# Kernel optimization log

Measured on AMD Instinct MI355X. Metric: run time of the kernel, lower is better.

Reference implementation:

```python
import jax, jax.numpy as jnp
import numpy as np

EPS = 1e-5


def _conv_w(x, k):
    # cross-correlation along width, kernel size 2, padding 1 -> width W+1
    xp = jnp.pad(x, ((0, 0), (0, 0), (0, 0), (1, 1)))
    return k[0] * xp[..., :-1] + k[1] * xp[..., 1:]


def _conv_h(x, k):
    # cross-correlation along height, kernel size 2, padding 1 -> height H+1
    xp = jnp.pad(x, ((0, 0), (0, 0), (1, 1), (0, 0)))
    return k[0] * xp[..., :-1, :] + k[1] * xp[..., 1:, :]


def _dwt(x, lp, hp):
    L = _conv_h(_conv_w(x, lp), lp)
    Hc = _conv_h(_conv_w(x, hp), hp)
    return L[:, :, ::2, ::2], Hc[:, :, ::2, ::2]


def _bn(y, g, b, m, v):
    # eval-mode batchnorm over channel axis 1
    scale = (g / jnp.sqrt(v + EPS))[None, :, None, None]
    shift = (b - m * g / jnp.sqrt(v + EPS))[None, :, None, None]
    return y * scale + shift


def setup_inputs() -> dict:
    key = jax.random.key(0)
    ks = jax.random.split(key, 8)
    S, B, H, W, C = 5, 8, 512, 512, 64
    x = jax.random.normal(ks[0], (B, 1, H, W), dtype=jnp.float32)
    lp = jnp.tile(jnp.array([0.7071, 0.7071], dtype=jnp.float32), (S, 1))
    hp = jnp.tile(jnp.array([0.7071, -0.7071], dtype=jnp.float32), (S, 1))
    w1 = jax.random.normal(ks[1], (S, C, 1), dtype=jnp.float32) * 0.5
    w2 = jax.random.normal(ks[2], (S, C, C), dtype=jnp.float32) * (1.0 / np.sqrt(C))
    g1 = jnp.ones((S, C), jnp.float32)
    b1 = jnp.zeros((S, C), jnp.float32)
    m1 = jax.random.normal(ks[3], (S, C), dtype=jnp.float32) * 0.1
    v1 = jax.random.uniform(ks[4], (S, C), dtype=jnp.float32) + 0.5
    g2 = jnp.ones((S, C), jnp.float32)
    b2 = jnp.zeros((S, C), jnp.float32)
    m2 = jax.random.normal(ks[5], (S, C), dtype=jnp.float32) * 0.1
    v2 = jax.random.uniform(ks[6], (S, C), dtype=jnp.float32) + 0.5
    return dict(x=x, lp=lp, hp=hp, w1=w1, w2=w2, g1=g1, b1=b1, m1=m1, v1=v1,
                g2=g2, b2=b2, m2=m2, v2=v2)


def reference(x, lp, hp, w1, w2, g1, b1, m1, v1, g2, b2, m2, v2):
    # Returns stacked-over-scale (L, H_coeff, processed_L):
    #   L, Hc: [S, B, 1, H', W'];  P: [S, B, 64, H', W']
    def per_scale(lp_s, hp_s, w1_s, g1_s, b1_s, m1_s, v1_s,
                  w2_s, g2_s, b2_s, m2_s, v2_s):
        L, Hc = _dwt(x, lp_s, hp_s)
        y = jnp.einsum('oc,bchw->bohw', w1_s, L)
        y = jax.nn.relu(_bn(y, g1_s, b1_s, m1_s, v1_s))
        y = jnp.einsum('oc,bchw->bohw', w2_s, y)
        y = jax.nn.relu(_bn(y, g2_s, b2_s, m2_s, v2_s))
        return L, Hc, y

    return jax.vmap(per_scale)(lp, hp, w1, g1, b1, m1, v1, w2, g2, b2, m2, v2)
```

## Files before the change

kernel.cpp:

```cpp
#include <hip/hip_runtime.h>
#include <math.h>

#define EPSF 1e-5f

constexpr int Sn = 5, Bn = 8, Hin = 512, Win = 512, Cn = 64;
constexpr int HO = 257, WO = 257;
constexpr int HW = HO * WO;
constexpr int NPIX = Bn * HW;
constexpr int TOTPIX = Sn * NPIX;

constexpr int WSF = 64 + Cn * 66 * 2;

__global__ __launch_bounds__(64) void precompute_kernel(
    const float* __restrict__ w1, const float* __restrict__ w2,
    const float* __restrict__ g1, const float* __restrict__ b1,
    const float* __restrict__ m1, const float* __restrict__ v1,
    const float* __restrict__ g2, const float* __restrict__ b2,
    const float* __restrict__ m2, const float* __restrict__ v2,
    float* __restrict__ ws) {
    int s = blockIdx.x;
    int c = threadIdx.x;
    __shared__ float sa1[Cn], st1[Cn], stc[Cn], stS[Cn];
    __shared__ int   scS[Cn];

    int idx = s * Cn + c;
    float sc1 = g1[idx] / sqrtf(v1[idx] + EPSF);
    float a1  = sc1 * w1[idx];
    float t1  = b1[idx] - m1[idx] * sc1;
    sa1[c] = a1;
    st1[c] = t1;
    float tc = (a1 != 0.f) ? (-t1 / a1) : INFINITY;
    stc[c] = tc;
    __syncthreads();

    int rk = 0;
    for (int c2 = 0; c2 < Cn; c2++) {
        float t = stc[c2];
        rk += (t < tc) || (t == tc && c2 < c);
    }
    stS[rk] = tc;
    scS[rk] = c;
    __syncthreads();

    float* wss = ws + (size_t)s * WSF;
    wss[c] = stS[c];

    int o = c;
    float sc2 = g2[idx] / sqrtf(v2[idx] + EPSF);
    float t2o = b2[idx] - m2[idx] * sc2;
    const float* w2row = w2 + ((size_t)s * Cn + o) * Cn;

    float alpha = 0.f, beta = t2o;
    for (int cc = 0; cc < Cn; cc++) {
        float a = sa1[cc];
        bool act = (a < 0.f) || (a == 0.f && st1[cc] > 0.f);
        if (act) {
            float wf = sc2 * w2row[cc];
            alpha = fmaf(wf, a, alpha);
            beta  = fmaf(wf, st1[cc], beta);
        }
    }
    float2* abrow = (float2*)(wss + Cn);
    abrow[o * 66 + 0] = make_float2(alpha, beta);

    for (int r = 1; r <= Cn; r++) {
        int cc = scS[r - 1];
        float a = sa1[cc];
        if (a != 0.f) {
            float wf = sc2 * w2row[cc];
            float sgn = (a > 0.f) ? 1.f : -1.f;
            alpha = fmaf(sgn * wf, a, alpha);
            beta  = fmaf(sgn * wf, st1[cc], beta);
        }
        abrow[o * 66 + r] = make_float2(alpha, beta);
    }
}

constexpr int PPT = 4;

__global__ __launch_bounds__(256) void fused_kernel(
    const float* __restrict__ x,
    const float* __restrict__ lp, const float* __restrict__ hp,
    const float* __restrict__ ws,
    float* __restrict__ Lout, float* __restrict__ Hout,
    float* __restrict__ Pout) {
    __shared__ float  stS[Cn];
    __shared__ float2 sab[Cn * 66];

    int tid = threadIdx.x;
    int s   = blockIdx.y;
    const float* wss = ws + (size_t)s * WSF;
    if (tid < Cn) stS[tid] = wss[tid];
    const float2* abg = (const float2*)(wss + Cn);
    for (int t = tid; t < Cn * 66; t += 256) sab[t] = abg[t];
    __syncthreads();

    float l0 = lp[2 * s], l1 = lp[2 * s + 1];
    float h0 = hp[2 * s], h1 = hp[2 * s + 1];

    for (int k = 0; k < PPT; k++) {
        int p = (blockIdx.x * PPT + k) * 256 + tid;
        if (p >= NPIX) return;
        int b  = p / HW;
        int hw = p - b * HW;
        int i  = hw / WO;
        int j  = hw - i * WO;

        int r0 = 2 * i - 1, r1 = 2 * i;
        int c0 = 2 * j - 1, c1 = 2 * j;
        const float* xb = x + (size_t)b * (Hin * Win);
        float x00 = (r0 >= 0  && c0 >= 0 ) ? xb[r0 * Win + c0] : 0.f;
        float x01 = (r0 >= 0  && c1 < Win) ? xb[r0 * Win + c1] : 0.f;
        float x10 = (r1 < Hin && c0 >= 0 ) ? xb[r1 * Win + c0] : 0.f;
        float x11 = (r1 < Hin && c1 < Win) ? xb[r1 * Win + c1] : 0.f;

        float Lv = l0 * (l0 * x00 + l1 * x01) + l1 * (l0 * x10 + l1 * x11);
        float Hv = h0 * (h0 * x00 + h1 * x01) + h1 * (h0 * x10 + h1 * x11);

        size_t gid = (size_t)s * NPIX + p;
        Lout[gid] = Lv;
        Hout[gid] = Hv;

        int lo = 0, hi = Cn;
        while (lo < hi) {
            int mid = (lo + hi) >> 1;
            if (stS[mid] < Lv) lo = mid + 1; else hi = mid;
        }

        float* Pp = Pout + ((size_t)(s * Bn + b) * Cn) * HW + hw;
        #pragma unroll 16
        for (int o = 0; o < Cn; o++) {
            float2 ab = sab[o * 66 + lo];
            Pp[(size_t)o * HW] = fmaxf(fmaf(ab.x, Lv, ab.y), 0.f);
        }
    }
}

extern "C" void kernel_launch(void* const* d_in, const int* in_sizes, int n_in,
                              void* d_out, int out_size, void* d_ws, size_t ws_size,
                              hipStream_t stream) {
    const float* x  = (const float*)d_in[0];
    const float* lp = (const float*)d_in[1];
    const float* hp = (const float*)d_in[2];
    const float* w1 = (const float*)d_in[3];
    const float* w2 = (const float*)d_in[4];
    const float* g1 = (const float*)d_in[5];
    const float* b1 = (const float*)d_in[6];
    const float* m1 = (const float*)d_in[7];
    const float* v1 = (const float*)d_in[8];
    const float* g2 = (const float*)d_in[9];
    const float* b2 = (const float*)d_in[10];
    const float* m2 = (const float*)d_in[11];
    const float* v2 = (const float*)d_in[12];

    float* out  = (float*)d_out;
    float* Lout = out;
    float* Hout = out + TOTPIX;
    float* Pout = out + 2 * TOTPIX;
    float* ws   = (float*)d_ws;

    precompute_kernel<<<Sn, Cn, 0, stream>>>(w1, w2, g1, b1, m1, v1,
                                             g2, b2, m2, v2, ws);

    int blocksPerScale = (NPIX + 256 * PPT - 1) / (256 * PPT);
    dim3 grid(blocksPerScale, Sn);
    fused_kernel<<<grid, 256, 0, stream>>>(x, lp, hp, ws, Lout, Hout, Pout);
}
```

Before: 852.2 us.

## Vectorize output stores with float4 using per-channel alignment offsets

```diff
diff --git a/kernel.cpp b/kernel.cpp
--- a/kernel.cpp
+++ b/kernel.cpp
@@ -76,9 +76,16 @@
     }
 }
 
-constexpr int PPT = 4;
-
-__global__ __launch_bounds__(256) void fused_kernel(
+constexpr int GPT = 4;
+constexpr int TPB = 256;
+constexpr int PIXPB = TPB * GPT;
+constexpr int NCHUNK = (HW + PIXPB - 1) / PIXPB;
+
+__device__ __forceinline__ float pwl(const float2 ab, float v) {
+    return fmaxf(fmaf(ab.x, v, ab.y), 0.f);
+}
+
+__global__ __launch_bounds__(TPB) void fused_kernel(
     const float* __restrict__ x,
     const float* __restrict__ lp, const float* __restrict__ hp,
     const float* __restrict__ ws,
@@ -87,51 +94,126 @@
     __shared__ float  stS[Cn];
     __shared__ float2 sab[Cn * 66];
 
-    int tid = threadIdx.x;
-    int s   = blockIdx.y;
+    const int tid = threadIdx.x;
+    const int b = blockIdx.y, s = blockIdx.z;
     const float* wss = ws + (size_t)s * WSF;
     if (tid < Cn) stS[tid] = wss[tid];
     const float2* abg = (const float2*)(wss + Cn);
-    for (int t = tid; t < Cn * 66; t += 256) sab[t] = abg[t];
+    for (int t = tid; t < Cn * 66; t += TPB) sab[t] = abg[t];
     __syncthreads();
 
-    float l0 = lp[2 * s], l1 = lp[2 * s + 1];
-    float h0 = hp[2 * s], h1 = hp[2 * s + 1];
-
-    for (int k = 0; k < PPT; k++) {
-        int p = (blockIdx.x * PPT + k) * 256 + tid;
-        if (p >= NPIX) return;
-        int b  = p / HW;
-        int hw = p - b * HW;
-        int i  = hw / WO;
-        int j  = hw - i * WO;
-
-        int r0 = 2 * i - 1, r1 = 2 * i;
-        int c0 = 2 * j - 1, c1 = 2 * j;
-        const float* xb = x + (size_t)b * (Hin * Win);
-        float x00 = (r0 >= 0  && c0 >= 0 ) ? xb[r0 * Win + c0] : 0.f;
-        float x01 = (r0 >= 0  && c1 < Win) ? xb[r0 * Win + c1] : 0.f;
-        float x10 = (r1 < Hin && c0 >= 0 ) ? xb[r1 * Win + c0] : 0.f;
-        float x11 = (r1 < Hin && c1 < Win) ? xb[r1 * Win + c1] : 0.f;
-
-        float Lv = l0 * (l0 * x00 + l1 * x01) + l1 * (l0 * x10 + l1 * x11);
-        float Hv = h0 * (h0 * x00 + h1 * x01) + h1 * (h0 * x10 + h1 * x11);
-
-        size_t gid = (size_t)s * NPIX + p;
-        Lout[gid] = Lv;
-        Hout[gid] = Hv;
-
+    const int pbase = (blockIdx.x * TPB + tid) * GPT;
+    if (pbase >= HW) return;
+
+    const float l0 = lp[2 * s], l1 = lp[2 * s + 1];
+    const float h0 = hp[2 * s], h1 = hp[2 * s + 1];
+    const float* xb = x + (size_t)b * (Hin * Win);
+
+    float Lv[GPT + 3];
+    float Hv[GPT];
+    int   lo7[GPT + 3];
+
+    #pragma unroll
+    for (int q = 0; q < GPT + 3; ++q) {
+        const int px = pbase + q;
+        float Lq = 0.f, Hq = 0.f;
+        if (px < HW) {
+            const int i = px / WO;
+            const int j = px - i * WO;
+            const int r0 = 2 * i - 1, r1 = 2 * i;
+            const int c0 = 2 * j - 1, c1 = 2 * j;
+            const float x00 = (r0 >= 0  && c0 >= 0 ) ? xb[r0 * Win + c0] : 0.f;
+            const float x01 = (r0 >= 0  && c1 < Win) ? xb[r0 * Win + c1] : 0.f;
+            const float x10 = (r1 < Hin && c0 >= 0 ) ? xb[r1 * Win + c0] : 0.f;
+            const float x11 = (r1 < Hin && c1 < Win) ? xb[r1 * Win + c1] : 0.f;
+            Lq = l0 * (l0 * x00 + l1 * x01) + l1 * (l0 * x10 + l1 * x11);
+            Hq = h0 * (h0 * x00 + h1 * x01) + h1 * (h0 * x10 + h1 * x11);
+        }
+        Lv[q] = Lq;
+        if (q < GPT) Hv[q] = Hq;
         int lo = 0, hi = Cn;
         while (lo < hi) {
-            int mid = (lo + hi) >> 1;
-            if (stS[mid] < Lv) lo = mid + 1; else hi = mid;
-        }
-
-        float* Pp = Pout + ((size_t)(s * Bn + b) * Cn) * HW + hw;
-        #pragma unroll 16
-        for (int o = 0; o < Cn; o++) {
-            float2 ab = sab[o * 66 + lo];
-            Pp[(size_t)o * HW] = fmaxf(fmaf(ab.x, Lv, ab.y), 0.f);
+            const int mid = (lo + hi) >> 1;
+            if (stS[mid] < Lq) lo = mid + 1; else hi = mid;
+        }
+        lo7[q] = lo;
+    }
+
+    {
+        const size_t lbase = (size_t)(s * Bn + b) * HW + pbase;
+        #pragma unroll
+        for (int q = 0; q < GPT; ++q) {
+            if (pbase + q < HW) {
+                Lout[lbase + q] = Lv[q];
+                Hout[lbase + q] = Hv[q];
+            }
+        }
+    }
+
+    float* const Pb = Pout + ((size_t)(s * Bn + b) * Cn) * HW + pbase;
+
+    if (pbase + GPT + 3 <= HW) {
+        float* po = Pb;
+        #pragma unroll 2
+        for (int o = 0; o < Cn; o += 4, po += (size_t)4 * HW) {
+            {
+                const float2 a0 = sab[o * 66 + lo7[0]];
+                const float2 a1 = sab[o * 66 + lo7[1]];
+                const float2 a2 = sab[o * 66 + lo7[2]];
+                const float2 a3 = sab[o * 66 + lo7[3]];
+                const float4 v = make_float4(pwl(a0, Lv[0]), pwl(a1, Lv[1]),
+                                             pwl(a2, Lv[2]), pwl(a3, Lv[3]));
+                *(float4*)(po) = v;
+            }
+            {
+                const float2 a0 = sab[(o + 1) * 66 + lo7[3]];
+                const float2 a1 = sab[(o + 1) * 66 + lo7[4]];
+                const float2 a2 = sab[(o + 1) * 66 + lo7[5]];
+                const float2 a3 = sab[(o + 1) * 66 + lo7[6]];
+                const float4 v = make_float4(pwl(a0, Lv[3]), pwl(a1, Lv[4]),
+                                             pwl(a2, Lv[5]), pwl(a3, Lv[6]));
+                *(float4*)(po + HW + 3) = v;
+            }
+            {
+                const float2 a0 = sab[(o + 2) * 66 + lo7[2]];
+                const float2 a1 = sab[(o + 2) * 66 + lo7[3]];
+                const float2 a2 = sab[(o + 2) * 66 + lo7[4]];
+                const float2 a3 = sab[(o + 2) * 66 + lo7[5]];
+                const float4 v = make_float4(pwl(a0, Lv[2]), pwl(a1, Lv[3]),
+                                             pwl(a2, Lv[4]), pwl(a3, Lv[5]));
+                *(float4*)(po + 2 * (size_t)HW + 2) = v;
+            }
+            {
+                const float2 a0 = sab[(o + 3) * 66 + lo7[1]];
+                const float2 a1 = sab[(o + 3) * 66 + lo7[2]];
+                const float2 a2 = sab[(o + 3) * 66 + lo7[3]];
+                const float2 a3 = sab[(o + 3) * 66 + lo7[4]];
+                const float4 v = make_float4(pwl(a0, Lv[1]), pwl(a1, Lv[2]),
+                                             pwl(a2, Lv[3]), pwl(a3, Lv[4]));
+                *(float4*)(po + 3 * (size_t)HW + 1) = v;
+            }
+        }
+        if (pbase == 0) {
+            float* ph = Pb;
+            for (int o = 0; o < Cn; ++o, ph += HW) {
+                const int d = (4 - (o & 3)) & 3;
+                if (d > 0) ph[0] = pwl(sab[o * 66 + lo7[0]], Lv[0]);
+                if (d > 1) ph[1] = pwl(sab[o * 66 + lo7[1]], Lv[1]);
+                if (d > 2) ph[2] = pwl(sab[o * 66 + lo7[2]], Lv[2]);
+            }
+        }
+    } else {
+        #pragma unroll
+        for (int q = 0; q < GPT; ++q) {
+            const int px = pbase + q;
+            if (px >= HW) break;
+            const float Lq = Lv[q];
+            const int   r  = lo7[q];
+            float* Pp = Pb + q;
+            #pragma unroll 8
+            for (int o = 0; o < Cn; ++o) {
+                Pp[(size_t)o * HW] = pwl(sab[o * 66 + r], Lq);
+            }
         }
     }
 }
@@ -162,7 +244,6 @@
     precompute_kernel<<<Sn, Cn, 0, stream>>>(w1, w2, g1, b1, m1, v1,
                                              g2, b2, m2, v2, ws);
 
-    int blocksPerScale = (NPIX + 256 * PPT - 1) / (256 * PPT);
-    dim3 grid(blocksPerScale, Sn);
-    fused_kernel<<<grid, 256, 0, stream>>>(x, lp, hp, ws, Lout, Hout, Pout);
-}
+    dim3 grid(NCHUNK, Bn, Sn);
+    fused_kernel<<<grid, TPB, 0, stream>>>(x, lp, hp, ws, Lout, Hout, Pout);
+}
```

Result: faster. 789.3 us (-7.4%).
